# Kernel tuning notes

Measured on AMD Instinct MI355X. Metric: run time of the kernel, lower is better.

The kernel has to match this reference:

```python
import jax, jax.numpy as jnp
import numpy as np

HEADS = 10
HEAD_DIM = 64
ATTN_SCALE = HEAD_DIM ** -0.5
SHARED_SCORE_SHIFT = 0.6931472  # ln(2)
SHARED_SCORE_SCALE = 1.0
EPS = 1e-5


def expand_first(feat, scale=1.0):
    # feat: [b, ...]; broadcast style stats from batch 0 and b//2 over each half
    b = feat.shape[0]
    style = jnp.stack([feat[0], feat[b // 2]])[:, None]          # [2, 1, ...]
    style = jnp.broadcast_to(style, (2, b // 2) + feat.shape[1:])
    if scale != 1.0:
        factors = jnp.where(jnp.arange(b // 2) == 0, 1.0, scale)
        factors = factors.reshape((1, b // 2) + (1,) * (feat.ndim - 1))
        style = style * factors
    return style.reshape(feat.shape)


def adain(feat):
    # stats over the sequence axis (dim=-2); torch .var() is unbiased (ddof=1)
    mean = jnp.mean(feat, axis=-2, keepdims=True)
    std = jnp.sqrt(jnp.var(feat, axis=-2, keepdims=True, ddof=1) + EPS)
    style_mean = expand_first(mean)
    style_std = expand_first(std)
    return (feat - mean) / std * style_std + style_mean


def setup_inputs() -> dict:
    key = jax.random.key(0)
    B, N, C = 4, 2048, 640
    ks = jax.random.split(key, 6)
    hidden_states = jax.random.normal(ks[0], (B, N, C), dtype=jnp.float32)
    w_scale = 0.03
    wq = jax.random.normal(ks[1], (C, C), dtype=jnp.float32) * w_scale
    wk = jax.random.normal(ks[2], (C, C), dtype=jnp.float32) * w_scale
    wv = jax.random.normal(ks[3], (C, C), dtype=jnp.float32) * w_scale
    wo = jax.random.normal(ks[4], (C, C), dtype=jnp.float32) * w_scale
    bo = jnp.zeros((C,), dtype=jnp.float32)
    return {"hidden_states": hidden_states, "wq": wq, "wk": wk, "wv": wv, "wo": wo, "bo": bo}


def reference(hidden_states, wq, wk, wv, wo, bo):
    b, n, c = hidden_states.shape
    # to_q / to_k / to_v (bias-free Linear: y = x @ W^T)
    q = hidden_states @ wq.T
    k = hidden_states @ wk.T
    v = hidden_states @ wv.T
    # [b, heads, n, head_dim]
    q = q.reshape(b, n, HEADS, HEAD_DIM).transpose(0, 2, 1, 3)
    k = k.reshape(b, n, HEADS, HEAD_DIM).transpose(0, 2, 1, 3)
    v = v.reshape(b, n, HEADS, HEAD_DIM).transpose(0, 2, 1, 3)
    # AdaIN on queries and keys (adain_values=False)
    q = adain(q)
    k = adain(k)
    # cross-batch KV style sharing
    k = expand_first(k, SHARED_SCORE_SCALE)
    v = expand_first(v, SHARED_SCORE_SCALE)
    # shifted scaled-dot-product attention: shift added to logit columns >= Nq
    logits = jnp.einsum('bhqd,bhkd->bhqk', q, k) * ATTN_SCALE
    nq, nk = q.shape[2], k.shape[2]
    shift = SHARED_SCORE_SHIFT * (jnp.arange(nk) >= nq).astype(logits.dtype)
    logits = logits + shift  # no-op here since nk == nq, kept for fidelity
    probs = jax.nn.softmax(logits, axis=-1)
    out = jnp.einsum('bhqk,bhkd->bhqd', probs, v)
    # merge heads, output projection (to_out[0] Linear + to_out[1] Dropout=identity)
    out = out.transpose(0, 2, 1, 3).reshape(b, n, HEADS * HEAD_DIM)
    out = out @ wo.T + bo
    # residual connection, rescale_output_factor = 1
    return out + hidden_states
```

## Files before the change

### kernel.cpp

```cpp
#include <hip/hip_runtime.h>
#include <hip/hip_bf16.h>
#include <math.h>

#define Bb 4
#define Nn 2048
#define Cc 640
#define Hh 10
#define Dd 64
#define EPSf 1e-5f
#define QSCALE 0.18033688f
#define KVT 64

typedef __attribute__((ext_vector_type(8))) short bf16x8;
typedef __attribute__((ext_vector_type(4))) float f32x4;
typedef __attribute__((ext_vector_type(16))) float f32x16;
typedef __attribute__((ext_vector_type(8))) unsigned short u16x8;
typedef __attribute__((ext_vector_type(4))) unsigned int u32x4;
typedef __attribute__((ext_vector_type(2))) unsigned int u32x2v;

__device__ inline unsigned short f2bf(float f) {
    unsigned int x = __float_as_uint(f);
    unsigned int r = (x + 0x7fffu + ((x >> 16) & 1u)) >> 16;
    return (unsigned short)r;
}
__device__ inline float bf2f(unsigned short v) {
    return __uint_as_float(((unsigned int)v) << 16);
}
__device__ inline unsigned pkbf(float a, float b) {
    __hip_bfloat162 t = __float22bfloat162_rn(float2{a, b});
    union { __hip_bfloat162 h; unsigned u; } cv; cv.h = t;
    return cv.u;
}
__device__ inline unsigned cvtpk(float lo, float hi) {
    unsigned r;
    asm("v_cvt_pk_bf16_f32 %0, %1, %2" : "=v"(r) : "v"(lo), "v"(hi));
    return r;
}
__device__ inline f32x4 mfma16(bf16x8 a, bf16x8 b, f32x4 c) {
    return __builtin_amdgcn_mfma_f32_16x16x32_bf16(a, b, c, 0, 0, 0);
}
__device__ inline f32x16 mfma32(bf16x8 a, bf16x8 b, f32x16 c) {
    return __builtin_amdgcn_mfma_f32_32x32x16_bf16(a, b, c, 0, 0, 0);
}
__device__ inline void gl16(const ushort* g, char* l) {
    __builtin_amdgcn_global_load_lds(
        (const __attribute__((address_space(1))) unsigned int*)g,
        (__attribute__((address_space(3))) unsigned int*)l, 16, 0, 0);
}

__global__ __launch_bounds__(256)
void tobf16_all(const float* __restrict__ hs, const float* __restrict__ wq,
                const float* __restrict__ wk, const float* __restrict__ wv,
                const float* __restrict__ wo,
                ushort* __restrict__ Xb, ushort* __restrict__ Wqb,
                ushort* __restrict__ Wkb, ushort* __restrict__ Wvb,
                ushort* __restrict__ Wob) {
    const int bid = blockIdx.x;
    const float* src;
    ushort* dst;
    int i;
    if (bid < 2560) {
        src = hs; dst = Xb; i = bid * 256 + threadIdx.x;
    } else {
        int w = (bid - 2560) / 200;
        int rb = (bid - 2560) % 200;
        src = (w == 0) ? wq : (w == 1) ? wk : (w == 2) ? wv : wo;
        dst = (w == 0) ? Wqb : (w == 1) ? Wkb : (w == 2) ? Wvb : Wob;
        i = rb * 256 + threadIdx.x;
    }
    const size_t base = (size_t)i * 8;
    float4 a = *reinterpret_cast<const float4*>(src + base);
    float4 b = *reinterpret_cast<const float4*>(src + base + 4);
    u16x8 o;
    o[0] = f2bf(a.x); o[1] = f2bf(a.y); o[2] = f2bf(a.z); o[3] = f2bf(a.w);
    o[4] = f2bf(b.x); o[5] = f2bf(b.y); o[6] = f2bf(b.z); o[7] = f2bf(b.w);
    *reinterpret_cast<u16x8*>(dst + base) = o;
}

template<int MODE>
__device__ __forceinline__ void gemm_body(
    const ushort* __restrict__ X, const ushort* __restrict__ W,
    ushort* __restrict__ outh, float* __restrict__ outf,
    const float* __restrict__ bo, const float* __restrict__ hs,
    int mt, int h, char* As, char* Bs)
{
    const int tid = threadIdx.x;
    const int wv = tid >> 6, lane = tid & 63;
    const int c = lane & 15, g = lane >> 4;
    const int r0 = mt * 128;
    const int xr0 = (MODE == 1 || MODE == 2) ? (r0 < Nn ? r0 : r0 + Nn) : r0;
    const int o0 = h * 64;

    const int grow = lane >> 3;
    const int gcol = ((((lane & 7) * 16) ^ ((lane >> 3) << 4)) >> 1);

    f32x4 acc[2][4];
    #pragma unroll
    for (int i = 0; i < 2; ++i)
        #pragma unroll
        for (int j = 0; j < 4; ++j)
            acc[i][j] = (f32x4){0.f, 0.f, 0.f, 0.f};

    for (int k0 = 0; k0 < Cc; k0 += 64) {
        __syncthreads();
        #pragma unroll
        for (int i = 0; i < 4; ++i) {
            int a = wv * 4 + i;
            gl16(X + (size_t)(xr0 + a * 8 + grow) * Cc + k0 + gcol, As + a * 1024);
        }
        #pragma unroll
        for (int i = 0; i < 2; ++i) {
            int bb = wv * 2 + i;
            gl16(W + (size_t)(o0 + bb * 8 + grow) * Cc + k0 + gcol, Bs + bb * 1024);
        }
        __syncthreads();

        bf16x8 xf[2][2], wf[4][2];
        #pragma unroll
        for (int rt = 0; rt < 2; ++rt) {
            int row = wv * 32 + rt * 16 + c;
            #pragma unroll
            for (int ks = 0; ks < 2; ++ks)
                xf[rt][ks] = *reinterpret_cast<const bf16x8*>(
                    As + row * 128 + ((ks * 64 + g * 16) ^ ((row & 7) << 4)));
        }
        #pragma unroll
        for (int ct = 0; ct < 4; ++ct) {
            int row = ct * 16 + c;
            #pragma unroll
            for (int ks = 0; ks < 2; ++ks)
                wf[ct][ks] = *reinterpret_cast<const bf16x8*>(
                    Bs + row * 128 + ((ks * 64 + g * 16) ^ ((row & 7) << 4)));
        }
        #pragma unroll
        for (int rt = 0; rt < 2; ++rt)
            #pragma unroll
            for (int ct = 0; ct < 4; ++ct)
                #pragma unroll
                for (int ks = 0; ks < 2; ++ks) {
                    if constexpr (MODE == 2)
                        acc[rt][ct] = mfma16(xf[rt][ks], wf[ct][ks], acc[rt][ct]);
                    else
                        acc[rt][ct] = mfma16(wf[ct][ks], xf[rt][ks], acc[rt][ct]);
                }
    }

    if constexpr (MODE == 0 || MODE == 1) {
        #pragma unroll
        for (int rt = 0; rt < 2; ++rt) {
            int r = r0 + wv * 32 + rt * 16 + c;
            int bi = r >> 11, n = r & 2047;
            #pragma unroll
            for (int ct = 0; ct < 4; ++ct) {
                int d0 = ct * 16 + g * 4;
                ushort4 v4;
                v4.x = f2bf(acc[rt][ct][0]); v4.y = f2bf(acc[rt][ct][1]);
                v4.z = f2bf(acc[rt][ct][2]); v4.w = f2bf(acc[rt][ct][3]);
                *reinterpret_cast<ushort4*>(&outh[(((size_t)(bi * Hh + h)) * Nn + n) * Dd + d0]) = v4;
            }
        }
    } else if constexpr (MODE == 2) {
        #pragma unroll
        for (int rt = 0; rt < 2; ++rt) {
            int r = r0 + wv * 32 + rt * 16 + g * 4;
            int kb = r >> 11, n = r & 2047;
            #pragma unroll
            for (int ct = 0; ct < 4; ++ct) {
                int d = ct * 16 + c;
                ushort4 v4;
                v4.x = f2bf(acc[rt][ct][0]); v4.y = f2bf(acc[rt][ct][1]);
                v4.z = f2bf(acc[rt][ct][2]); v4.w = f2bf(acc[rt][ct][3]);
                *reinterpret_cast<ushort4*>(&outh[(((size_t)(kb * Hh + h)) * Dd + d) * Nn + n]) = v4;
            }
        }
    } else {
        #pragma unroll
        for (int rt = 0; rt < 2; ++rt) {
            int r = r0 + wv * 32 + rt * 16 + c;
            #pragma unroll
            for (int ct = 0; ct < 4; ++ct) {
                int o = h * 64 + ct * 16 + g * 4;
                float4 bvv = *reinterpret_cast<const float4*>(&bo[o]);
                float4 hv = *reinterpret_cast<const float4*>(&hs[(size_t)r * Cc + o]);
                float4 ov;
                ov.x = acc[rt][ct][0] + bvv.x + hv.x;
                ov.y = acc[rt][ct][1] + bvv.y + hv.y;
                ov.z = acc[rt][ct][2] + bvv.z + hv.z;
                ov.w = acc[rt][ct][3] + bvv.w + hv.w;
                *reinterpret_cast<float4*>(&outf[(size_t)r * Cc + o]) = ov;
            }
        }
    }
}

__global__ __launch_bounds__(256)
void gemm_qkv(const ushort* __restrict__ X, const ushort* __restrict__ Wq,
              const ushort* __restrict__ Wk, const ushort* __restrict__ Wv,
              ushort* __restrict__ Qh, ushort* __restrict__ K16,
              ushort* __restrict__ Vt16) {
    __shared__ alignas(16) char As[16384];
    __shared__ alignas(16) char Bs[8192];
    const int bx = blockIdx.x;
    if (bx < 64)
        gemm_body<0>(X, Wq, Qh, nullptr, nullptr, nullptr, bx, blockIdx.y, As, Bs);
    else if (bx < 96)
        gemm_body<1>(X, Wk, K16, nullptr, nullptr, nullptr, bx - 64, blockIdx.y, As, Bs);
    else
        gemm_body<2>(X, Wv, Vt16, nullptr, nullptr, nullptr, bx - 96, blockIdx.y, As, Bs);
}

__global__ __launch_bounds__(256)
void gemm_out(const ushort* __restrict__ Ain, const ushort* __restrict__ Wo,
              float* __restrict__ out, const float* __restrict__ bo,
              const float* __restrict__ hs) {
    __shared__ alignas(16) char As[16384];
    __shared__ alignas(16) char Bs[8192];
    gemm_body<3>(Ain, Wo, nullptr, out, bo, hs, blockIdx.x, blockIdx.y, As, Bs);
}

__global__ __launch_bounds__(256)
void stats_kernel(const ushort* __restrict__ Q, float* __restrict__ mean, float* __restrict__ stdv) {
    const int bh = blockIdx.x;
    const int tid = threadIdx.x;
    const int doct = tid & 7, ng = tid >> 3;
    const ushort* base = Q + (size_t)bh * Nn * Dd + (size_t)ng * Dd + doct * 8;
    float s[8] = {}, ss[8] = {};
    for (int it = 0; it < 64; ++it) {
        u16x8 v = *reinterpret_cast<const u16x8*>(base + (size_t)it * 32 * Dd);
        #pragma unroll
        for (int j = 0; j < 8; ++j) {
            float x = bf2f(v[j]);
            s[j] += x; ss[j] += x * x;
        }
    }
    __shared__ float S[32][64], SS[32][64];
    #pragma unroll
    for (int j = 0; j < 8; ++j) {
        S[ng][doct * 8 + j] = s[j];
        SS[ng][doct * 8 + j] = ss[j];
    }
    __syncthreads();
    if (tid < 64) {
        float st = 0.f, sst = 0.f;
        #pragma unroll
        for (int gg = 0; gg < 32; ++gg) { st += S[gg][tid]; sst += SS[gg][tid]; }
        float mu = st / (float)Nn;
        float var = (sst - (float)Nn * mu * mu) / (float)(Nn - 1);
        mean[bh * 64 + tid] = mu;
        stdv[bh * 64 + tid] = sqrtf(var + EPSf);
    }
}

__global__ __launch_bounds__(512, 4)
void attn_mfma(const ushort* __restrict__ Qh, const float* __restrict__ mean,
               const float* __restrict__ stdv,
               const ushort* __restrict__ Kb, const ushort* __restrict__ Vtb,
               ushort* __restrict__ Ao) {
    __shared__ alignas(16) char smem[32768];
    __shared__ float lsh[8][32];

    const int tid = threadIdx.x;
    const int wid = tid >> 6, lane = tid & 63;
    const int half = wid >> 2, wq = wid & 3;
    const int q31 = lane & 31, hi = lane >> 5;
    const int bh = blockIdx.x, b = bh / Hh, h = bh % Hh, kb = b >> 1;
    const int qw0 = blockIdx.y * 128 + wq * 32;
    const int kv0 = half * (Nn / 2);

    char* Ksh = smem + half * 8192;
    char* Vsh = smem + 16384 + half * 8192;

    const ushort* qp = Qh + ((size_t)bh * Nn + qw0) * Dd;
    const ushort* kp = Kb + ((size_t)(kb * Hh + h) * Nn + kv0) * Dd;
    const ushort* vp = Vtb + ((size_t)(kb * Hh + h)) * Dd * Nn + kv0;

    bf16x8 qf[4];
    #pragma unroll
    for (int dsl = 0; dsl < 4; ++dsl) {
        const int d0 = dsl * 16 + hi * 8;
        u16x8 qin = *reinterpret_cast<const u16x8*>(qp + (size_t)q31 * Dd + d0);
        float x[8];
        #pragma unroll
        for (int j = 0; j < 8; ++j) x[j] = bf2f(qin[j]);
        if (b & 1) {
            const float* mS = mean + bh * 64 + d0;
            const float* sS = stdv + bh * 64 + d0;
            const float* mT = mean + (bh - Hh) * 64 + d0;
            const float* sT = stdv + (bh - Hh) * 64 + d0;
            #pragma unroll
            for (int j = 0; j < 8; ++j) {
                float r = sT[j] / sS[j];
                x[j] = (x[j] * r + (mT[j] - mS[j] * r)) * QSCALE;
            }
        } else {
            #pragma unroll
            for (int j = 0; j < 8; ++j) x[j] *= QSCALE;
        }
        u32x4 pw = {pkbf(x[0], x[1]), pkbf(x[2], x[3]), pkbf(x[4], x[5]), pkbf(x[6], x[7])};
        qf[dsl] = *reinterpret_cast<bf16x8*>(&pw);
    }

    f32x16 acc0, acc1;
    #pragma unroll
    for (int r = 0; r < 16; ++r) { acc0[r] = 0.f; acc1[r] = 0.f; }
    float l = 0.f;

    const int htid = tid & 255;
    const int srow = htid >> 3, sch = htid & 7;
    const int swz = (sch * 16) ^ ((srow & 7) << 4);
    const int soff0 = srow * 128 + swz;
    const int soff1 = (srow + 32) * 128 + swz;
    const ushort* kg0 = kp + (size_t)srow * Dd + sch * 8;
    const ushort* kg1 = kp + (size_t)(srow + 32) * Dd + sch * 8;
    const ushort* vg0 = vp + (size_t)srow * Nn + sch * 8;
    const ushort* vg1 = vp + (size_t)(srow + 32) * Nn + sch * 8;

    bf16x8 kr0 = *reinterpret_cast<const bf16x8*>(kg0);
    bf16x8 kr1 = *reinterpret_cast<const bf16x8*>(kg1);
    bf16x8 vr0 = *reinterpret_cast<const bf16x8*>(vg0);
    bf16x8 vr1 = *reinterpret_cast<const bf16x8*>(vg1);
    *reinterpret_cast<bf16x8*>(Ksh + soff0) = kr0;
    *reinterpret_cast<bf16x8*>(Ksh + soff1) = kr1;
    *reinterpret_cast<bf16x8*>(Vsh + soff0) = vr0;
    *reinterpret_cast<bf16x8*>(Vsh + soff1) = vr1;
    __syncthreads();

    const int kx = (q31 & 7) << 4;

    for (int kt = 0; kt < Nn / 2; kt += KVT) {
        const bool has_next = (kt + KVT) < (Nn / 2);
        if (has_next) {
            kr0 = *reinterpret_cast<const bf16x8*>(kg0 + (size_t)(kt + KVT) * Dd);
            kr1 = *reinterpret_cast<const bf16x8*>(kg1 + (size_t)(kt + KVT) * Dd);
            vr0 = *reinterpret_cast<const bf16x8*>(vg0 + kt + KVT);
            vr1 = *reinterpret_cast<const bf16x8*>(vg1 + kt + KVT);
        }

        f32x16 st0, st1;
        #pragma unroll
        for (int r = 0; r < 16; ++r) { st0[r] = 0.f; st1[r] = 0.f; }
        #pragma unroll
        for (int dsl = 0; dsl < 4; ++dsl) {
            bf16x8 kf0 = *reinterpret_cast<const bf16x8*>(
                Ksh + q31 * 128 + ((dsl * 32 + hi * 16) ^ kx));
            bf16x8 kf1 = *reinterpret_cast<const bf16x8*>(
                Ksh + (q31 + 32) * 128 + ((dsl * 32 + hi * 16) ^ kx));
            st0 = mfma32(kf0, qf[dsl], st0);
            st1 = mfma32(kf1, qf[dsl], st1);
        }

        #pragma unroll
        for (int r = 0; r < 16; ++r) st0[r] = __builtin_amdgcn_exp2f(st0[r]);
        #pragma unroll
        for (int r = 0; r < 16; ++r) st1[r] = __builtin_amdgcn_exp2f(st1[r]);

        {
            float s2[16];
            #pragma unroll
            for (int r = 0; r < 16; ++r) s2[r] = st0[r] + st1[r];
            float s4[8];
            #pragma unroll
            for (int r = 0; r < 8; ++r) s4[r] = s2[r] + s2[r + 8];
            float s8[4];
            #pragma unroll
            for (int r = 0; r < 4; ++r) s8[r] = s4[r] + s4[r + 4];
            l += (s8[0] + s8[1]) + (s8[2] + s8[3]);
        }

        #pragma unroll
        for (int kvm = 0; kvm < 2; ++kvm) {
            #pragma unroll
            for (int tt = 0; tt < 2; ++tt) {
                float p0, p1, p2, p3, p4, p5, p6, p7;
                if (kvm == 0) {
                    p0 = st0[8*tt+0]; p1 = st0[8*tt+1]; p2 = st0[8*tt+2]; p3 = st0[8*tt+3];
                    p4 = st0[8*tt+4]; p5 = st0[8*tt+5]; p6 = st0[8*tt+6]; p7 = st0[8*tt+7];
                } else {
                    p0 = st1[8*tt+0]; p1 = st1[8*tt+1]; p2 = st1[8*tt+2]; p3 = st1[8*tt+3];
                    p4 = st1[8*tt+4]; p5 = st1[8*tt+5]; p6 = st1[8*tt+6]; p7 = st1[8*tt+7];
                }
                unsigned a0 = cvtpk(p0, p1);
                unsigned a1 = cvtpk(p2, p3);
                unsigned b0 = cvtpk(p4, p5);
                unsigned b1 = cvtpk(p6, p7);
                u32x2v r0 = __builtin_amdgcn_permlane32_swap(a0, b0, false, false);
                u32x2v r1 = __builtin_amdgcn_permlane32_swap(a1, b1, false, false);
                u32x4 fw = {r0[0], r1[0], r0[1], r1[1]};
                bf16x8 pf = *reinterpret_cast<bf16x8*>(&fw);
                const int km = kvm * 2 + tt;
                bf16x8 vf0 = *reinterpret_cast<const bf16x8*>(
                    Vsh + q31 * 128 + ((km * 32 + hi * 16) ^ kx));
                bf16x8 vf1 = *reinterpret_cast<const bf16x8*>(
                    Vsh + (q31 + 32) * 128 + ((km * 32 + hi * 16) ^ kx));
                acc0 = mfma32(pf, vf0, acc0);
                acc1 = mfma32(pf, vf1, acc1);
            }
        }

        if (has_next) {
            __syncthreads();
            *reinterpret_cast<bf16x8*>(Ksh + soff0) = kr0;
            *reinterpret_cast<bf16x8*>(Ksh + soff1) = kr1;
            *reinterpret_cast<bf16x8*>(Vsh + soff0) = vr0;
            *reinterpret_cast<bf16x8*>(Vsh + soff1) = vr1;
            __syncthreads();
        }
    }

    l += __shfl_xor(l, 32);
    lsh[wid][q31] = l;
    __syncthreads();
    float* fs = (float*)smem;
    if (half == 1) {
        float* dst = fs + wq * 2048;
        #pragma unroll
        for (int r = 0; r < 16; ++r) {
            dst[r * 64 + lane] = acc0[r];
            dst[(16 + r) * 64 + lane] = acc1[r];
        }
    }
    __syncthreads();
    if (half == 0) {
        const float* src = fs + wq * 2048;
        float ltot = l + lsh[wid + 4][q31];
        float inv = 1.0f / ltot;
        #pragma unroll
        for (int r = 0; r < 16; ++r) {
            const int qlr = (r & 3) + 8 * (r >> 2) + 4 * hi;
            float o0 = (acc0[r] + src[r * 64 + lane]) * inv;
            float o1 = (acc1[r] + src[(16 + r) * 64 + lane]) * inv;
            size_t o = (size_t)(b * Nn + qw0 + qlr) * Cc + h * Dd + q31;
            Ao[o]      = f2bf(o0);
            Ao[o + 32] = f2bf(o1);
        }
    }
}

extern "C" void kernel_launch(void* const* d_in, const int* in_sizes, int n_in,
                              void* d_out, int out_size, void* d_ws, size_t ws_size,
                              hipStream_t stream) {
    const float* hs = (const float*)d_in[0];
    const float* wq = (const float*)d_in[1];
    const float* wk = (const float*)d_in[2];
    const float* wv = (const float*)d_in[3];
    const float* wo = (const float*)d_in[4];
    const float* bo = (const float*)d_in[5];
    float* out = (float*)d_out;

    ushort* Xb   = (ushort*)d_ws;
    ushort* Wqb  = Xb + 5242880;
    ushort* Wkb  = Wqb + 409600;
    ushort* Wvb  = Wkb + 409600;
    ushort* Wob  = Wvb + 409600;
    ushort* Qh   = Wob + 409600;
    ushort* K16  = Qh + 5242880;
    ushort* Vt16 = K16 + 2621440;
    ushort* Aob  = Vt16 + 2621440;
    float*  mean = (float*)(Aob + 5242880);
    float*  stdv = mean + 2560;

    tobf16_all<<<3360, 256, 0, stream>>>(hs, wq, wk, wv, wo, Xb, Wqb, Wkb, Wvb, Wob);

    gemm_qkv<<<dim3(128, 10), 256, 0, stream>>>(Xb, Wqb, Wkb, Wvb, Qh, K16, Vt16);
    stats_kernel<<<40, 256, 0, stream>>>(Qh, mean, stdv);
    attn_mfma<<<dim3(40, 16), 512, 0, stream>>>(Qh, mean, stdv, K16, Vt16, Aob);
    gemm_out<<<dim3(64, 10), 256, 0, stream>>>(Aob, Wob, out, bo, hs);
}
```

Before: 122.0 us.

## Fuse Q AdaIN statistics into QKV GEMM epilogue and drop stats kernel

The Q projection GEMM epilogue now reduces per-column sums and sums of squares over its 128-row tile and writes partial statistics to a buffer. The attention kernel combines the 16 partials per batch-head into mean and std in shared memory, so the separate stats kernel and its re-read of Q are gone. The attention loop also raises wave priority around the MFMA sections. Statistics are now taken from fp32 accumulators rather than bf16-rounded Q, and the GEMM gains a small reduction epilogue.

```diff
diff --git a/kernel.cpp b/kernel.cpp
--- a/kernel.cpp
+++ b/kernel.cpp
@@ -82,6 +82,7 @@
     const ushort* __restrict__ X, const ushort* __restrict__ W,
     ushort* __restrict__ outh, float* __restrict__ outf,
     const float* __restrict__ bo, const float* __restrict__ hs,
+    float* __restrict__ Pstats,
     int mt, int h, char* As, char* Bs)
 {
     const int tid = threadIdx.x;
@@ -191,22 +192,57 @@
             }
         }
     }
+
+    if constexpr (MODE == 0) {
+        __syncthreads();
+        float* Sw  = (float*)As;
+        float* Sw2 = (float*)(As + 1024);
+        #pragma unroll
+        for (int ct = 0; ct < 4; ++ct) {
+            #pragma unroll
+            for (int rg = 0; rg < 4; ++rg) {
+                float a0 = acc[0][ct][rg], a1 = acc[1][ct][rg];
+                float v = a0 + a1;
+                float q = a0 * a0 + a1 * a1;
+                #pragma unroll
+                for (int m = 1; m < 16; m <<= 1) {
+                    v += __shfl_xor(v, m);
+                    q += __shfl_xor(q, m);
+                }
+                if (c == 0) {
+                    int d = ct * 16 + g * 4 + rg;
+                    Sw[wv * 64 + d] = v;
+                    Sw2[wv * 64 + d] = q;
+                }
+            }
+        }
+        __syncthreads();
+        if (tid < 64) {
+            float s = Sw[tid] + Sw[64 + tid] + Sw[128 + tid] + Sw[192 + tid];
+            float q = Sw2[tid] + Sw2[64 + tid] + Sw2[128 + tid] + Sw2[192 + tid];
+            int bi = mt >> 4, slot = mt & 15;
+            int bh = bi * Hh + h;
+            float* p = Pstats + ((size_t)(bh * 16 + slot) * 2) * 64;
+            p[tid] = s;
+            p[64 + tid] = q;
+        }
+    }
 }
 
 __global__ __launch_bounds__(256)
 void gemm_qkv(const ushort* __restrict__ X, const ushort* __restrict__ Wq,
               const ushort* __restrict__ Wk, const ushort* __restrict__ Wv,
               ushort* __restrict__ Qh, ushort* __restrict__ K16,
-              ushort* __restrict__ Vt16) {
+              ushort* __restrict__ Vt16, float* __restrict__ Pstats) {
     __shared__ alignas(16) char As[16384];
     __shared__ alignas(16) char Bs[8192];
     const int bx = blockIdx.x;
     if (bx < 64)
-        gemm_body<0>(X, Wq, Qh, nullptr, nullptr, nullptr, bx, blockIdx.y, As, Bs);
+        gemm_body<0>(X, Wq, Qh, nullptr, nullptr, nullptr, Pstats, bx, blockIdx.y, As, Bs);
     else if (bx < 96)
-        gemm_body<1>(X, Wk, K16, nullptr, nullptr, nullptr, bx - 64, blockIdx.y, As, Bs);
+        gemm_body<1>(X, Wk, K16, nullptr, nullptr, nullptr, nullptr, bx - 64, blockIdx.y, As, Bs);
     else
-        gemm_body<2>(X, Wv, Vt16, nullptr, nullptr, nullptr, bx - 96, blockIdx.y, As, Bs);
+        gemm_body<2>(X, Wv, Vt16, nullptr, nullptr, nullptr, nullptr, bx - 96, blockIdx.y, As, Bs);
 }
 
 __global__ __launch_bounds__(256)
@@ -215,49 +251,16 @@
               const float* __restrict__ hs) {
     __shared__ alignas(16) char As[16384];
     __shared__ alignas(16) char Bs[8192];
-    gemm_body<3>(Ain, Wo, nullptr, out, bo, hs, blockIdx.x, blockIdx.y, As, Bs);
-}
-
-__global__ __launch_bounds__(256)
-void stats_kernel(const ushort* __restrict__ Q, float* __restrict__ mean, float* __restrict__ stdv) {
-    const int bh = blockIdx.x;
-    const int tid = threadIdx.x;
-    const int doct = tid & 7, ng = tid >> 3;
-    const ushort* base = Q + (size_t)bh * Nn * Dd + (size_t)ng * Dd + doct * 8;
-    float s[8] = {}, ss[8] = {};
-    for (int it = 0; it < 64; ++it) {
-        u16x8 v = *reinterpret_cast<const u16x8*>(base + (size_t)it * 32 * Dd);
-        #pragma unroll
-        for (int j = 0; j < 8; ++j) {
-            float x = bf2f(v[j]);
-            s[j] += x; ss[j] += x * x;
-        }
-    }
-    __shared__ float S[32][64], SS[32][64];
-    #pragma unroll
-    for (int j = 0; j < 8; ++j) {
-        S[ng][doct * 8 + j] = s[j];
-        SS[ng][doct * 8 + j] = ss[j];
-    }
-    __syncthreads();
-    if (tid < 64) {
-        float st = 0.f, sst = 0.f;
-        #pragma unroll
-        for (int gg = 0; gg < 32; ++gg) { st += S[gg][tid]; sst += SS[gg][tid]; }
-        float mu = st / (float)Nn;
-        float var = (sst - (float)Nn * mu * mu) / (float)(Nn - 1);
-        mean[bh * 64 + tid] = mu;
-        stdv[bh * 64 + tid] = sqrtf(var + EPSf);
-    }
+    gemm_body<3>(Ain, Wo, nullptr, out, bo, hs, nullptr, blockIdx.x, blockIdx.y, As, Bs);
 }
 
 __global__ __launch_bounds__(512, 4)
-void attn_mfma(const ushort* __restrict__ Qh, const float* __restrict__ mean,
-               const float* __restrict__ stdv,
+void attn_mfma(const ushort* __restrict__ Qh, const float* __restrict__ Pstats,
                const ushort* __restrict__ Kb, const ushort* __restrict__ Vtb,
                ushort* __restrict__ Ao) {
     __shared__ alignas(16) char smem[32768];
     __shared__ float lsh[8][32];
+    __shared__ float statl[4][64];
 
     const int tid = threadIdx.x;
     const int wid = tid >> 6, lane = tid & 63;
@@ -274,6 +277,27 @@
     const ushort* kp = Kb + ((size_t)(kb * Hh + h) * Nn + kv0) * Dd;
     const ushort* vp = Vtb + ((size_t)(kb * Hh + h)) * Dd * Nn + kv0;
 
+    if (b & 1) {
+        if (tid < 128) {
+            const int which = tid >> 6;
+            const int d = tid & 63;
+            const int tb = which ? (bh - Hh) : bh;
+            const float* p = Pstats + ((size_t)(tb * 16) * 2) * 64;
+            float s = 0.f, q = 0.f;
+            #pragma unroll
+            for (int j = 0; j < 16; ++j) {
+                s += p[(j * 2) * 64 + d];
+                q += p[(j * 2 + 1) * 64 + d];
+            }
+            float mu = s / (float)Nn;
+            float var = (q - (float)Nn * mu * mu) / (float)(Nn - 1);
+            float sd = sqrtf(var + EPSf);
+            statl[which * 2 + 0][d] = mu;
+            statl[which * 2 + 1][d] = sd;
+        }
+        __syncthreads();
+    }
+
     bf16x8 qf[4];
     #pragma unroll
     for (int dsl = 0; dsl < 4; ++dsl) {
@@ -283,14 +307,10 @@
         #pragma unroll
         for (int j = 0; j < 8; ++j) x[j] = bf2f(qin[j]);
         if (b & 1) {
-            const float* mS = mean + bh * 64 + d0;
-            const float* sS = stdv + bh * 64 + d0;
-            const float* mT = mean + (bh - Hh) * 64 + d0;
-            const float* sT = stdv + (bh - Hh) * 64 + d0;
             #pragma unroll
             for (int j = 0; j < 8; ++j) {
-                float r = sT[j] / sS[j];
-                x[j] = (x[j] * r + (mT[j] - mS[j] * r)) * QSCALE;
+                float r = statl[3][d0 + j] / statl[1][d0 + j];
+                x[j] = (x[j] * r + (statl[2][d0 + j] - statl[0][d0 + j] * r)) * QSCALE;
             }
         } else {
             #pragma unroll
@@ -339,6 +359,7 @@
         f32x16 st0, st1;
         #pragma unroll
         for (int r = 0; r < 16; ++r) { st0[r] = 0.f; st1[r] = 0.f; }
+        __builtin_amdgcn_s_setprio(1);
         #pragma unroll
         for (int dsl = 0; dsl < 4; ++dsl) {
             bf16x8 kf0 = *reinterpret_cast<const bf16x8*>(
@@ -348,6 +369,7 @@
             st0 = mfma32(kf0, qf[dsl], st0);
             st1 = mfma32(kf1, qf[dsl], st1);
         }
+        __builtin_amdgcn_s_setprio(0);
 
         #pragma unroll
         for (int r = 0; r < 16; ++r) st0[r] = __builtin_amdgcn_exp2f(st0[r]);
@@ -367,6 +389,7 @@
             l += (s8[0] + s8[1]) + (s8[2] + s8[3]);
         }
 
+        __builtin_amdgcn_s_setprio(1);
         #pragma unroll
         for (int kvm = 0; kvm < 2; ++kvm) {
             #pragma unroll
@@ -396,6 +419,7 @@
                 acc1 = mfma32(pf, vf1, acc1);
             }
         }
+        __builtin_amdgcn_s_setprio(0);
 
         if (has_next) {
             __syncthreads();
@@ -456,13 +480,11 @@
     ushort* K16  = Qh + 5242880;
     ushort* Vt16 = K16 + 2621440;
     ushort* Aob  = Vt16 + 2621440;
-    float*  mean = (float*)(Aob + 5242880);
-    float*  stdv = mean + 2560;
+    float*  Pstats = (float*)(Aob + 5242880);
 
     tobf16_all<<<3360, 256, 0, stream>>>(hs, wq, wk, wv, wo, Xb, Wqb, Wkb, Wvb, Wob);
 
-    gemm_qkv<<<dim3(128, 10), 256, 0, stream>>>(Xb, Wqb, Wkb, Wvb, Qh, K16, Vt16);
-    stats_kernel<<<40, 256, 0, stream>>>(Qh, mean, stdv);
-    attn_mfma<<<dim3(40, 16), 512, 0, stream>>>(Qh, mean, stdv, K16, Vt16, Aob);
+    gemm_qkv<<<dim3(128, 10), 256, 0, stream>>>(Xb, Wqb, Wkb, Wvb, Qh, K16, Vt16, Pstats);
+    attn_mfma<<<dim3(40, 16), 512, 0, stream>>>(Qh, Pstats, K16, Vt16, Aob);
     gemm_out<<<dim3(64, 10), 256, 0, stream>>>(Aob, Wob, out, bo, hs);
 }
```

Measured after the change: 130.8 us. +7.2%, slower.
